# Performance work log

Hardware: AMD Instinct MI355X
Metric: run time of the kernel (lower is better)

The kernel has to match this reference:

```python
import jax, jax.numpy as jnp
import numpy as np

ALPHA = 2.0  # init kwarg alpha


def _edt(mask):
    """Exact Euclidean distance from each pixel to the nearest False pixel.
    mask: (H, W) bool. Matches scipy.ndimage.distance_transform_edt(mask).
    Separable algorithm: 1D L1 pass along columns, then exact min over columns.
    """
    H, W = mask.shape
    INF = jnp.float32(H + W)
    g0 = jnp.where(mask, INF, 0.0).astype(jnp.float32)  # 0 at background pixels

    def step(carry, row):
        g = jnp.minimum(row, carry + 1.0)
        return g, g

    _, fwd = jax.lax.scan(step, jnp.full((W,), INF, jnp.float32), g0)
    _, bwd = jax.lax.scan(step, jnp.full((W,), INF, jnp.float32), fwd[::-1])
    g = bwd[::-1]  # (H, W): vertical distance to nearest bg in same column

    j = jnp.arange(W, dtype=jnp.float32)
    d2 = (j[:, None] - j[None, :]) ** 2  # (Wj, Wk)
    # dist2[i, j] = min_k g[i, k]^2 + (j - k)^2   -> exact squared EDT
    dist2 = jnp.min(g[:, None, :] ** 2 + d2[None, :, :], axis=-1)  # (H, W)
    return jnp.sqrt(dist2)


def _distance_field(img):
    """img: (N, H, W) float. Replicates LogHausdorffDTLoss.distance_field per slice."""

    def one(ch):
        mask = ch > 0.5
        valid = jnp.logical_and(mask.any(), ~mask.all())
        field = _edt(mask) + _edt(~mask)  # fg_dist + bg_dist
        return jnp.where(valid, field, 0.0)

    # sequential map keeps peak memory to one (H, W, W) intermediate at a time
    return jax.lax.map(one, img)


def setup_inputs() -> dict:
    key = jax.random.key(0)
    k1, k2, k3 = jax.random.split(key, 3)
    B, C, H, W = 8, 4, 256, 256
    preds_S = jax.random.normal(k1, (B, C, H, W), dtype=jnp.float32)
    preds_T = jax.random.normal(k2, (B, C, H, W), dtype=jnp.float32)
    target = jax.random.uniform(k3, (B, 1, H, W), dtype=jnp.float32)
    return {"preds_S": preds_S, "preds_T": preds_T, "target": target}


def reference(preds_S, preds_T, target):
    # shapes already match -> no interpolation; sigmoid=False, softmax=True, C>1
    C = preds_S.shape[1]
    p = jax.nn.softmax(preds_S, axis=1)

    # to_onehot_y=True: target is overwritten by onehot(argmax(teacher)) (detached)
    pT = jax.lax.stop_gradient(preds_T)
    labels = jnp.argmax(pT, axis=1)  # (B, H, W)
    tgt = jax.nn.one_hot(labels, C, axis=1, dtype=p.dtype)  # (B, C, H, W)

    # include_background=False: drop channel 0
    p = p[:, 1:]
    tgt = tgt[:, 1:]
    B, Cc, H, W = p.shape

    pred_dt = _distance_field(jax.lax.stop_gradient(p).reshape(-1, H, W)).reshape(B, Cc, H, W)
    tgt_dt = _distance_field(tgt.reshape(-1, H, W)).reshape(B, Cc, H, W)
    pred_dt = jax.lax.stop_gradient(pred_dt)
    tgt_dt = jax.lax.stop_gradient(tgt_dt)

    err = (p - tgt) ** 2
    dist = pred_dt ** ALPHA + tgt_dt ** ALPHA
    # per-channel means all cover B*H*W elements -> mean of means == global mean
    loss = jnp.mean(err * dist)
    return jnp.log(loss + 1.0)
```

## Files before the change

kernel.cpp:

```cpp
#include <hip/hip_runtime.h>
#include <math.h>

#define HWTOT 65536
#define WD 256
#define HT 256
#define NSL 24

static constexpr size_t OFF_CNT  = 0;
static constexpr size_t OFF_PART = 256;
static constexpr size_t OFF_PCNT = 24832;
static constexpr size_t OFF_MASK = 49408;
static constexpr size_t OFF_ERR  = OFF_MASK + (size_t)NSL * HWTOT;
static constexpr size_t OFF_G    = OFF_ERR + (size_t)NSL * HWTOT * 2;

__global__ __launch_bounds__(256) void k_mask(
    const float* __restrict__ pS, const float* __restrict__ pT,
    unsigned char* __restrict__ mask, _Float16* __restrict__ err,
    unsigned short* __restrict__ pcnt)
{
    __shared__ int lc[6];
    if (threadIdx.x < 6) lc[threadIdx.x] = 0;
    __syncthreads();

    int blk = blockIdx.x;
    int b   = blk >> 8;
    int lb  = blk & 255;
    int hw  = lb * 256 + threadIdx.x;

    const float* ps = pS + (size_t)b * 4 * HWTOT + hw;
    float s0 = ps[0], s1 = ps[HWTOT], s2 = ps[2 * HWTOT], s3 = ps[3 * HWTOT];
    float mx = fmaxf(fmaxf(s0, s1), fmaxf(s2, s3));
    float e0 = expf(s0 - mx), e1 = expf(s1 - mx), e2 = expf(s2 - mx), e3 = expf(s3 - mx);
    float inv = 1.0f / (e0 + e1 + e2 + e3);

    const float* pt = pT + (size_t)b * 4 * HWTOT + hw;
    float t0 = pt[0], t1 = pt[HWTOT], t2 = pt[2 * HWTOT], t3 = pt[3 * HWTOT];
    int lab = 0; float bm = t0;
    if (t1 > bm) { bm = t1; lab = 1; }
    if (t2 > bm) { bm = t2; lab = 2; }
    if (t3 > bm) { bm = t3; lab = 3; }

    float pv[3] = { e1 * inv, e2 * inv, e3 * inv };
    #pragma unroll
    for (int cc = 0; cc < 3; ++cc) {
        int sl = b * 3 + cc;
        bool mp = pv[cc] > 0.5f;
        bool mt = (lab == cc + 1);
        mask[(size_t)sl * HWTOT + hw] = (unsigned char)((mp ? 1 : 0) | (mt ? 2 : 0));
        float tcv = mt ? 1.0f : 0.0f;
        float ev = (pv[cc] - tcv) * (pv[cc] - tcv);
        err[(size_t)sl * HWTOT + hw] = (_Float16)ev;
        unsigned long long balP = __ballot(mp);
        unsigned long long balT = __ballot(mt);
        if ((threadIdx.x & 63) == 0) {
            atomicAdd(&lc[cc],     (int)__popcll(balP));
            atomicAdd(&lc[3 + cc], (int)__popcll(balT));
        }
    }
    __syncthreads();
    if (threadIdx.x < 3) {
        int sl = b * 3 + threadIdx.x;
        pcnt[(size_t)sl * 256 + lb] = (unsigned short)lc[threadIdx.x];
    } else if (threadIdx.x < 6) {
        int sl = b * 3 + (threadIdx.x - 3);
        pcnt[(size_t)(NSL + sl) * 256 + lb] = (unsigned short)lc[threadIdx.x];
    }
}

__global__ __launch_bounds__(256, 1) void k_vert(
    const unsigned char* __restrict__ mask, const unsigned short* __restrict__ pcnt,
    unsigned short* __restrict__ g, int* __restrict__ cnts)
{
    int s = blockIdx.x;
    int f = blockIdx.y;
    int w = threadIdx.x;

    const unsigned char* m = mask + (size_t)s * HWTOT + w;
    unsigned short* go = g + ((size_t)f * NSL + s) * HWTOT + w;

    unsigned up[128];
    unsigned mb32[8];
    int prevm = -1, d = 512;
    #pragma unroll
    for (int hb = 0; hb < 16; ++hb) {
        unsigned char mraw[16];
        #pragma unroll
        for (int i = 0; i < 16; ++i) mraw[i] = m[(hb * 16 + i) * WD];
        #pragma unroll
        for (int i = 0; i < 16; ++i) {
            int h = hb * 16 + i;
            int mv = (mraw[i] >> f) & 1;
            d = (prevm < 0) ? 512 : ((mv != prevm) ? 1 : min(d + 1, 512));
            prevm = mv;
            if (h & 1) up[h >> 1] |= (unsigned)d << 16;
            else       up[h >> 1]  = (unsigned)d;
            if ((h & 31) == 0) mb32[h >> 5]  = (unsigned)mv;
            else               mb32[h >> 5] |= (unsigned)mv << (h & 31);
        }
    }
    int nextm = -1; d = 512;
    #pragma unroll
    for (int hb = 15; hb >= 0; --hb) {
        unsigned short outv[16];
        #pragma unroll
        for (int i = 15; i >= 0; --i) {
            int h = hb * 16 + i;
            int mv = (mb32[h >> 5] >> (h & 31)) & 1;
            d = (nextm < 0) ? 512 : ((mv != nextm) ? 1 : min(d + 1, 512));
            nextm = mv;
            unsigned pk = up[h >> 1];
            int du = (h & 1) ? (int)(pk >> 16) : (int)(pk & 0xffffu);
            outv[i] = (unsigned short)min(du, d);
        }
        #pragma unroll
        for (int i = 0; i < 16; ++i) go[(hb * 16 + i) * WD] = outv[i];
    }

    __shared__ int cr[4];
    int v = (int)pcnt[((size_t)f * NSL + s) * 256 + w];
    #pragma unroll
    for (int i = 1; i < 64; i <<= 1) v += __shfl_xor(v, i);
    if ((w & 63) == 0) cr[w >> 6] = v;
    __syncthreads();
    if (w == 0) cnts[f * NSL + s] = cr[0] + cr[1] + cr[2] + cr[3];
}

__global__ __launch_bounds__(256) void k_row(
    const _Float16* __restrict__ err, const unsigned short* __restrict__ gAll,
    const unsigned char* __restrict__ mask,
    const int* __restrict__ cnts, float* __restrict__ partials)
{
    int h  = blockIdx.x;
    int s  = blockIdx.y;
    int jo = threadIdx.x;

    __shared__ float4 g2[768];
    __shared__ float  wred[4];

    const size_t fstride = (size_t)NSL * HWTOT;
    size_t rbase = (size_t)s * HWTOT + h * WD + jo;

    int gcP = gAll[rbase];
    int gcT = gAll[fstride + rbase];
    int mb  = mask[rbase];
    bool selP = mb & 1;
    bool selT = (mb >> 1) & 1;

    int cp = cnts[s];
    int ct = cnts[NSL + s];
    bool validP = (cp > 0) && (cp < HWTOT);
    bool validT = (ct > 0) && (ct < HWTOT);

    float fP = (float)(gcP * gcP);
    float fT = (float)(gcT * gcT);
    g2[256 + jo] = make_float4(selP ? fP : 0.0f, selP ? 0.0f : fP,
                               selT ? fT : 0.0f, selT ? 0.0f : fT);
    float4 inf4 = make_float4(1e30f, 1e30f, 1e30f, 1e30f);
    g2[jo] = inf4;
    g2[512 + jo] = inf4;

    int gsp = validP ? gcP : 0;
    int gst = validT ? gcT : 0;
    int R = min(max(gsp, gst), 256);
    #pragma unroll
    for (int i = 1; i < 64; i <<= 1) R = max(R, __shfl_xor(R, i));

    float m1 = (float)(gsp * gsp);
    float m2 = (float)(gst * gst);
    __syncthreads();

    for (int dd = 1; dd < R; ++dd) {
        float4 L  = g2[256 + jo - dd];
        float4 Rv = g2[256 + jo + dd];
        float d2 = (float)(dd * dd);
        float c1 = fminf(selP ? L.x : L.y, selP ? Rv.x : Rv.y);
        float c2 = fminf(selT ? L.z : L.w, selT ? Rv.z : Rv.w);
        m1 = fminf(m1, c1 + d2);
        m2 = fminf(m2, c2 + d2);
    }

    float contrib = (float)err[rbase] * (m1 + m2);

    #pragma unroll
    for (int off = 32; off > 0; off >>= 1) contrib += __shfl_down(contrib, off);
    if ((jo & 63) == 0) wred[jo >> 6] = contrib;
    __syncthreads();
    if (jo == 0) partials[s * 256 + h] = wred[0] + wred[1] + wred[2] + wred[3];
}

__global__ __launch_bounds__(256) void k_final(
    const float* __restrict__ partials, float* __restrict__ out)
{
    __shared__ double red[256];
    int t = threadIdx.x;
    double acc = 0.0;
    for (int i = t; i < NSL * 256; i += 256) acc += (double)partials[i];
    red[t] = acc;
    __syncthreads();
    for (int off = 128; off > 0; off >>= 1) {
        if (t < off) red[t] += red[t + off];
        __syncthreads();
    }
    if (t == 0) {
        double loss = red[0] / (double)((size_t)NSL * HWTOT);
        out[0] = (float)log(loss + 1.0);
    }
}

extern "C" void kernel_launch(void* const* d_in, const int* in_sizes, int n_in,
                              void* d_out, int out_size, void* d_ws, size_t ws_size,
                              hipStream_t stream)
{
    const float* pS = (const float*)d_in[0];
    const float* pT = (const float*)d_in[1];
    float* out = (float*)d_out;

    char* ws = (char*)d_ws;
    int*            cnts  = (int*)(ws + OFF_CNT);
    float*          parts = (float*)(ws + OFF_PART);
    unsigned short* pcnt  = (unsigned short*)(ws + OFF_PCNT);
    unsigned char*  mask  = (unsigned char*)(ws + OFF_MASK);
    _Float16*       err   = (_Float16*)(ws + OFF_ERR);
    unsigned short* gAll  = (unsigned short*)(ws + OFF_G);

    k_mask <<<dim3(2048),     dim3(256), 0, stream>>>(pS, pT, mask, err, pcnt);
    k_vert <<<dim3(NSL, 2),   dim3(256), 0, stream>>>(mask, pcnt, gAll, cnts);
    k_row  <<<dim3(256, NSL), dim3(256), 0, stream>>>(err, gAll, mask, cnts, parts);
    k_final<<<dim3(1),        dim3(256), 0, stream>>>(parts, out);
}
```

Before: 112.5 us.

## Replace vertical distance scan with column bitmasks and per-row ffs/clz search

The sequential forward/backward column scan kernel, which wrote 16-bit vertical distances, is replaced by a packing kernel. It compresses each column's fg/tgt masks into 8 32-bit words per column and computes slice counts with popc. The row kernel rebuilds each pixel's vertical distance on the fly by searching those bitmasks with ffs/clz, which removes the large g buffer write and read. The cost is extra ALU work in every row block (16 word loads and two 8-step bit searches per pixel, per field). The pack kernel has only 24 blocks doing strided byte loads, while the old vertical kernel had 48.

```diff
diff --git a/kernel.cpp b/kernel.cpp
--- a/kernel.cpp
+++ b/kernel.cpp
@@ -8,24 +8,17 @@
 
 static constexpr size_t OFF_CNT  = 0;
 static constexpr size_t OFF_PART = 256;
-static constexpr size_t OFF_PCNT = 24832;
-static constexpr size_t OFF_MASK = 49408;
+static constexpr size_t OFF_MASK = 24832;
 static constexpr size_t OFF_ERR  = OFF_MASK + (size_t)NSL * HWTOT;
-static constexpr size_t OFF_G    = OFF_ERR + (size_t)NSL * HWTOT * 2;
+static constexpr size_t OFF_BITS = OFF_ERR + (size_t)NSL * HWTOT * 2;
 
 __global__ __launch_bounds__(256) void k_mask(
     const float* __restrict__ pS, const float* __restrict__ pT,
-    unsigned char* __restrict__ mask, _Float16* __restrict__ err,
-    unsigned short* __restrict__ pcnt)
-{
-    __shared__ int lc[6];
-    if (threadIdx.x < 6) lc[threadIdx.x] = 0;
-    __syncthreads();
-
+    unsigned char* __restrict__ mask, _Float16* __restrict__ err)
+{
     int blk = blockIdx.x;
     int b   = blk >> 8;
-    int lb  = blk & 255;
-    int hw  = lb * 256 + threadIdx.x;
+    int hw  = (blk & 255) * 256 + threadIdx.x;
 
     const float* ps = pS + (size_t)b * 4 * HWTOT + hw;
     float s0 = ps[0], s1 = ps[HWTOT], s2 = ps[2 * HWTOT], s3 = ps[3 * HWTOT];
@@ -50,84 +43,72 @@
         float tcv = mt ? 1.0f : 0.0f;
         float ev = (pv[cc] - tcv) * (pv[cc] - tcv);
         err[(size_t)sl * HWTOT + hw] = (_Float16)ev;
-        unsigned long long balP = __ballot(mp);
-        unsigned long long balT = __ballot(mt);
-        if ((threadIdx.x & 63) == 0) {
-            atomicAdd(&lc[cc],     (int)__popcll(balP));
-            atomicAdd(&lc[3 + cc], (int)__popcll(balT));
+    }
+}
+
+__global__ __launch_bounds__(256) void k_pack(
+    const unsigned char* __restrict__ mask, unsigned* __restrict__ bits,
+    int* __restrict__ cnts)
+{
+    int s = blockIdx.x;
+    int w = threadIdx.x;
+    const unsigned char* m = mask + (size_t)s * HWTOT + w;
+
+    int cp = 0, ct = 0;
+    #pragma unroll
+    for (int k = 0; k < 8; ++k) {
+        unsigned vp = 0, vt = 0;
+        #pragma unroll
+        for (int i = 0; i < 32; ++i) {
+            unsigned v = m[(k * 32 + i) * WD];
+            vp |= (v & 1u) << i;
+            vt |= ((v >> 1) & 1u) << i;
         }
-    }
-    __syncthreads();
-    if (threadIdx.x < 3) {
-        int sl = b * 3 + threadIdx.x;
-        pcnt[(size_t)sl * 256 + lb] = (unsigned short)lc[threadIdx.x];
-    } else if (threadIdx.x < 6) {
-        int sl = b * 3 + (threadIdx.x - 3);
-        pcnt[(size_t)(NSL + sl) * 256 + lb] = (unsigned short)lc[threadIdx.x];
-    }
-}
-
-__global__ __launch_bounds__(256, 1) void k_vert(
-    const unsigned char* __restrict__ mask, const unsigned short* __restrict__ pcnt,
-    unsigned short* __restrict__ g, int* __restrict__ cnts)
-{
-    int s = blockIdx.x;
-    int f = blockIdx.y;
-    int w = threadIdx.x;
-
-    const unsigned char* m = mask + (size_t)s * HWTOT + w;
-    unsigned short* go = g + ((size_t)f * NSL + s) * HWTOT + w;
-
-    unsigned up[128];
-    unsigned mb32[8];
-    int prevm = -1, d = 512;
-    #pragma unroll
-    for (int hb = 0; hb < 16; ++hb) {
-        unsigned char mraw[16];
-        #pragma unroll
-        for (int i = 0; i < 16; ++i) mraw[i] = m[(hb * 16 + i) * WD];
-        #pragma unroll
-        for (int i = 0; i < 16; ++i) {
-            int h = hb * 16 + i;
-            int mv = (mraw[i] >> f) & 1;
-            d = (prevm < 0) ? 512 : ((mv != prevm) ? 1 : min(d + 1, 512));
-            prevm = mv;
-            if (h & 1) up[h >> 1] |= (unsigned)d << 16;
-            else       up[h >> 1]  = (unsigned)d;
-            if ((h & 31) == 0) mb32[h >> 5]  = (unsigned)mv;
-            else               mb32[h >> 5] |= (unsigned)mv << (h & 31);
-        }
-    }
-    int nextm = -1; d = 512;
-    #pragma unroll
-    for (int hb = 15; hb >= 0; --hb) {
-        unsigned short outv[16];
-        #pragma unroll
-        for (int i = 15; i >= 0; --i) {
-            int h = hb * 16 + i;
-            int mv = (mb32[h >> 5] >> (h & 31)) & 1;
-            d = (nextm < 0) ? 512 : ((mv != nextm) ? 1 : min(d + 1, 512));
-            nextm = mv;
-            unsigned pk = up[h >> 1];
-            int du = (h & 1) ? (int)(pk >> 16) : (int)(pk & 0xffffu);
-            outv[i] = (unsigned short)min(du, d);
-        }
-        #pragma unroll
-        for (int i = 0; i < 16; ++i) go[(hb * 16 + i) * WD] = outv[i];
-    }
-
-    __shared__ int cr[4];
-    int v = (int)pcnt[((size_t)f * NSL + s) * 256 + w];
-    #pragma unroll
-    for (int i = 1; i < 64; i <<= 1) v += __shfl_xor(v, i);
-    if ((w & 63) == 0) cr[w >> 6] = v;
-    __syncthreads();
-    if (w == 0) cnts[f * NSL + s] = cr[0] + cr[1] + cr[2] + cr[3];
+        bits[((size_t)(0 * NSL + s) * 8 + k) * WD + w] = vp;
+        bits[((size_t)(1 * NSL + s) * 8 + k) * WD + w] = vt;
+        cp += __popc(vp); ct += __popc(vt);
+    }
+
+    __shared__ int redc[8];
+    #pragma unroll
+    for (int i = 1; i < 64; i <<= 1) { cp += __shfl_xor(cp, i); ct += __shfl_xor(ct, i); }
+    if ((w & 63) == 0) { redc[w >> 6] = cp; redc[4 + (w >> 6)] = ct; }
+    __syncthreads();
+    if (w == 0) cnts[s]       = redc[0] + redc[1] + redc[2] + redc[3];
+    if (w == 1) cnts[NSL + s] = redc[4] + redc[5] + redc[6] + redc[7];
+}
+
+__device__ __forceinline__ int vdist(const unsigned W[8], unsigned inv, int h)
+{
+    int dd = 512;
+    #pragma unroll
+    for (int k = 0; k < 8; ++k) {
+        unsigned y = W[k] ^ inv;
+        unsigned gate;
+        if (k * 32 + 31 <= h)      gate = 0u;
+        else if (k * 32 > h)       gate = 0xFFFFFFFFu;
+        else                       gate = 0xFFFFFFFFu << ((h - k * 32) + 1);
+        unsigned z = y & gate;
+        int cand = k * 32 + (__ffs(z) - 1) - h;
+        dd = (z && dd == 512) ? cand : dd;
+    }
+    int du = 512;
+    #pragma unroll
+    for (int k = 7; k >= 0; --k) {
+        unsigned y = W[k] ^ inv;
+        unsigned gate;
+        if (k * 32 >= h)           gate = 0u;
+        else if (k * 32 + 32 <= h) gate = 0xFFFFFFFFu;
+        else                       gate = (1u << (h - k * 32)) - 1u;
+        unsigned z = y & gate;
+        int cand = h - (k * 32 + 31 - __clz(z));
+        du = (z && du == 512) ? cand : du;
+    }
+    return min(dd, du);
 }
 
 __global__ __launch_bounds__(256) void k_row(
-    const _Float16* __restrict__ err, const unsigned short* __restrict__ gAll,
-    const unsigned char* __restrict__ mask,
+    const _Float16* __restrict__ err, const unsigned* __restrict__ bits,
     const int* __restrict__ cnts, float* __restrict__ partials)
 {
     int h  = blockIdx.x;
@@ -137,14 +118,21 @@
     __shared__ float4 g2[768];
     __shared__ float  wred[4];
 
-    const size_t fstride = (size_t)NSL * HWTOT;
-    size_t rbase = (size_t)s * HWTOT + h * WD + jo;
-
-    int gcP = gAll[rbase];
-    int gcT = gAll[fstride + rbase];
-    int mb  = mask[rbase];
-    bool selP = mb & 1;
-    bool selT = (mb >> 1) & 1;
+    const unsigned* bP = bits + (size_t)(0 * NSL + s) * 8 * WD;
+    const unsigned* bT = bits + (size_t)(1 * NSL + s) * 8 * WD;
+    unsigned WP[8], WT[8];
+    #pragma unroll
+    for (int k = 0; k < 8; ++k) { WP[k] = bP[k * WD + jo]; WT[k] = bT[k * WD + jo]; }
+
+    int kh = h >> 5, r = h & 31;
+    unsigned mywP = 0, mywT = 0;
+    #pragma unroll
+    for (int k = 0; k < 8; ++k) if (k == kh) { mywP = WP[k]; mywT = WT[k]; }
+    bool selP = (mywP >> r) & 1;
+    bool selT = (mywT >> r) & 1;
+
+    int gcP = vdist(WP, selP ? 0xFFFFFFFFu : 0u, h);
+    int gcT = vdist(WT, selT ? 0xFFFFFFFFu : 0u, h);
 
     int cp = cnts[s];
     int ct = cnts[NSL + s];
@@ -179,6 +167,7 @@
         m2 = fminf(m2, c2 + d2);
     }
 
+    size_t rbase = (size_t)s * HWTOT + h * WD + jo;
     float contrib = (float)err[rbase] * (m1 + m2);
 
     #pragma unroll
@@ -218,13 +207,12 @@
     char* ws = (char*)d_ws;
     int*            cnts  = (int*)(ws + OFF_CNT);
     float*          parts = (float*)(ws + OFF_PART);
-    unsigned short* pcnt  = (unsigned short*)(ws + OFF_PCNT);
     unsigned char*  mask  = (unsigned char*)(ws + OFF_MASK);
     _Float16*       err   = (_Float16*)(ws + OFF_ERR);
-    unsigned short* gAll  = (unsigned short*)(ws + OFF_G);
-
-    k_mask <<<dim3(2048),     dim3(256), 0, stream>>>(pS, pT, mask, err, pcnt);
-    k_vert <<<dim3(NSL, 2),   dim3(256), 0, stream>>>(mask, pcnt, gAll, cnts);
-    k_row  <<<dim3(256, NSL), dim3(256), 0, stream>>>(err, gAll, mask, cnts, parts);
+    unsigned*       bits  = (unsigned*)(ws + OFF_BITS);
+
+    k_mask <<<dim3(2048),     dim3(256), 0, stream>>>(pS, pT, mask, err);
+    k_pack <<<dim3(NSL),      dim3(256), 0, stream>>>(mask, bits, cnts);
+    k_row  <<<dim3(256, NSL), dim3(256), 0, stream>>>(err, bits, cnts, parts);
     k_final<<<dim3(1),        dim3(256), 0, stream>>>(parts, out);
 }
```

Measured after the change: 113.6 us. Within noise of the previous version (+1.0%).
